# Performance work log

Hardware: AMD Instinct MI355X
Metric: run time of the kernel (lower is better)

The kernel has to match this reference:

```python
import jax, jax.numpy as jnp
import numpy as np

N = 50000   # nodes
E = 800000  # edges
D = 64      # attrs_dim
H = 128     # 2*attrs_dim (GIN MLP hidden)
L = 3       # gnn_layers_num
G = 128     # graphs in batch


def setup_inputs() -> dict:
    key = jax.random.key(0)
    ks = jax.random.split(key, 9)
    s = 0.1
    attrs = jax.random.normal(ks[0], (N, D), dtype=jnp.float32)
    edge_index = jax.random.randint(ks[1], (2, E), 0, N, dtype=jnp.int64)
    batch = jnp.sort(jax.random.randint(ks[2], (N,), 0, G, dtype=jnp.int64))
    W1 = jax.random.normal(ks[3], (L, D, H), dtype=jnp.float32) * s
    b1 = jnp.zeros((L, H), jnp.float32)
    W2 = jax.random.normal(ks[4], (L, H, H), dtype=jnp.float32) * s
    b2 = jnp.zeros((L, H), jnp.float32)
    W3 = jax.random.normal(ks[5], (L, H, D), dtype=jnp.float32) * s
    b3 = jnp.zeros((L, D), jnp.float32)
    return {"attrs": attrs, "W1": W1, "b1": b1, "W2": W2, "b2": b2,
            "W3": W3, "b3": b3, "edge_index": edge_index, "batch": batch}


def reference(attrs, W1, b1, W2, b2, W3, b3, edge_index, batch):
    src, dst = edge_index[0], edge_index[1]
    x = attrs
    for l in range(L):  # small fixed layer count
        # GINConv with eps=0: MLP(x + sum_{j->i} x_j)
        agg = jax.ops.segment_sum(x[src], dst, num_segments=N)
        h = x + agg
        # MLP with tanh after each linear (per MLP.forward)
        h = jnp.tanh(h @ W1[l] + b1[l])
        h = jnp.tanh(h @ W2[l] + b2[l])
        h = jnp.tanh(h @ W3[l] + b3[l])
        # outer activation in GNN.forward
        x = jnp.tanh(h)
    # scatter_mean over graph ids
    sums = jax.ops.segment_sum(x, batch, num_segments=G)          # [G, D]
    counts = jax.ops.segment_sum(jnp.ones((N,), x.dtype), batch, num_segments=G)
    return sums / jnp.maximum(counts, 1.0)[:, None]
```

## Files before the change

### kernel.cpp

```cpp
#include <hip/hip_runtime.h>
#include <math.h>

#define N_NODES 50000
#define N_EDGES 800000
#define DIM 64
#define HID 128
#define LAYERS 3
#define NGRAPH 128

#define SCAN_TILE 1024
#define SCAN_NB ((N_NODES + SCAN_TILE - 1) / SCAN_TILE)

#define POOL_ROWS 256
#define POOL_NB ((N_NODES + POOL_ROWS - 1) / POOL_ROWS)

typedef __attribute__((ext_vector_type(8))) short short8v;
typedef __attribute__((ext_vector_type(4))) float f32x4;

__device__ __forceinline__ float bf2f(unsigned short u) {
    return __uint_as_float(((unsigned)u) << 16);
}
__device__ __forceinline__ unsigned short f2bf(float x) {
    unsigned u = __float_as_uint(x);
    unsigned r = (u + 0x7fff + ((u >> 16) & 1)) >> 16;
    return (unsigned short)r;
}
__device__ __forceinline__ float fast_tanh(float x) {
    float xc = fminf(fmaxf(x, -9.0f), 9.0f);
    float y = __expf(2.0f * xc);
    return 1.0f - 2.0f * __builtin_amdgcn_rcpf(y + 1.0f);
}

__global__ void count_kernel(const int* __restrict__ dst,
                             int* __restrict__ counts,
                             int* __restrict__ rank) {
    int e = blockIdx.x * blockDim.x + threadIdx.x;
    if (e >= N_EDGES) return;
    rank[e] = atomicAdd(&counts[dst[e]], 1);
}

__global__ void scan_partial_kernel(const int* __restrict__ counts,
                                    int* __restrict__ bsum) {
    __shared__ int red[256];
    const int b = blockIdx.x, tid = threadIdx.x;
    const int base = b * SCAN_TILE + tid * 4;
    int s = 0;
    if (base + 3 < N_NODES) {
        int4 v = *reinterpret_cast<const int4*>(counts + base);
        s = v.x + v.y + v.z + v.w;
    } else {
        for (int i = 0; i < 4; ++i)
            if (base + i < N_NODES) s += counts[base + i];
    }
    red[tid] = s;
    __syncthreads();
    for (int off = 128; off > 0; off >>= 1) {
        if (tid < off) red[tid] += red[tid + off];
        __syncthreads();
    }
    if (tid == 0) bsum[b] = red[0];
}

__global__ void scan_mid_kernel(const int* __restrict__ bsum,
                                int* __restrict__ bpre,
                                int* __restrict__ offsets) {
    int tid = threadIdx.x;
    int orig = (tid < SCAN_NB) ? bsum[tid] : 0;
    int v = orig;
    for (int off = 1; off < 64; off <<= 1) {
        int u = __shfl_up(v, off);
        if (tid >= off) v += u;
    }
    if (tid < SCAN_NB) bpre[tid] = v - orig;
    if (tid == 0) offsets[N_NODES] = N_EDGES;
}

__global__ void scan_final_kernel(const int* __restrict__ counts,
                                  const int* __restrict__ bpre,
                                  int* __restrict__ offsets) {
    __shared__ int pre[256];
    const int b = blockIdx.x, tid = threadIdx.x;
    const int base = b * SCAN_TILE + tid * 4;
    int c[4];
    int s = 0;
#pragma unroll
    for (int i = 0; i < 4; ++i) {
        c[i] = (base + i < N_NODES) ? counts[base + i] : 0;
        s += c[i];
    }
    pre[tid] = s;
    __syncthreads();
    for (int off = 1; off < 256; off <<= 1) {
        int v = (tid >= off) ? pre[tid - off] : 0;
        __syncthreads();
        pre[tid] += v;
        __syncthreads();
    }
    int run = bpre[b] + pre[tid] - s;
#pragma unroll
    for (int i = 0; i < 4; ++i) {
        if (base + i < N_NODES) {
            offsets[base + i] = run;
            run += c[i];
        }
    }
}

__global__ void place_kernel(const int* __restrict__ src,
                             const int* __restrict__ dst,
                             const int* __restrict__ rank,
                             const int* __restrict__ offsets,
                             unsigned short* __restrict__ csr_src) {
    int e = blockIdx.x * blockDim.x + threadIdx.x;
    if (e >= N_EDGES) return;
    csr_src[offsets[dst[e]] + rank[e]] = (unsigned short)src[e];
}

template<int K, int C>
__global__ void repack_kernel(const float* __restrict__ W, unsigned short* __restrict__ P) {
    constexpr int KT = K / 32, CT = C / 16;
    int t = blockIdx.x * 256 + threadIdx.x;
    if (t >= LAYERS * KT * CT * 64) return;
    int lane = t & 63; int rest = t >> 6;
    int ct = rest % CT; rest /= CT;
    int kt = rest % KT; int l = rest / KT;
    int li = lane & 15, hi = lane >> 4;
    const float* Wl = W + (size_t)l * K * C;
    short8v o;
#pragma unroll
    for (int j = 0; j < 8; ++j)
        o[j] = (short)f2bf(Wl[(size_t)(kt * 32 + hi * 8 + j) * C + ct * 16 + li]);
    *reinterpret_cast<short8v*>(P + ((size_t)l * KT * CT * 64 + (size_t)(kt * CT + ct) * 64 + lane) * 8) = o;
}

template<bool F32IN>
__global__ __launch_bounds__(256) void gnn_layer_kernel(
        const float* __restrict__ xf, const unsigned short* __restrict__ xb,
        const int* __restrict__ offsets, const unsigned short* __restrict__ csr_src,
        const unsigned short* __restrict__ pw1, const float* __restrict__ bias1,
        const unsigned short* __restrict__ pw2, const float* __restrict__ bias2,
        const unsigned short* __restrict__ pw3, const float* __restrict__ bias3,
        unsigned short* __restrict__ outx) {
    __shared__ unsigned short agg[16 * 64];
    __shared__ unsigned short tileA[16 * 128];
    __shared__ unsigned short tileB[16 * 128];
    const int tid = threadIdx.x;
    const int wave = tid >> 6, lane = tid & 63;
    const int li = lane & 15, hi = lane >> 4;
    const int r0 = blockIdx.x * 16;
    char* tG = reinterpret_cast<char*>(agg);
    char* tA = reinterpret_cast<char*>(tileA);
    char* tB = reinterpret_cast<char*>(tileB);

    {
        const int nr = tid >> 4;
        const int q  = tid & 15;
        const int n  = r0 + nr;
        float a0, a1, a2, a3;
        if (F32IN) {
            float4 v = *reinterpret_cast<const float4*>(xf + (size_t)n * DIM + q * 4);
            a0 = v.x; a1 = v.y; a2 = v.z; a3 = v.w;
        } else {
            ushort4 v = *reinterpret_cast<const ushort4*>(xb + (size_t)n * DIM + q * 4);
            a0 = bf2f(v.x); a1 = bf2f(v.y); a2 = bf2f(v.z); a3 = bf2f(v.w);
        }
        int p = offsets[n];
        const int pe = offsets[n + 1];
        for (; p + 4 <= pe; p += 4) {
            int s0 = csr_src[p + 0];
            int s1 = csr_src[p + 1];
            int s2 = csr_src[p + 2];
            int s3 = csr_src[p + 3];
            if (F32IN) {
                float4 v0 = *reinterpret_cast<const float4*>(xf + (size_t)s0 * DIM + q * 4);
                float4 v1 = *reinterpret_cast<const float4*>(xf + (size_t)s1 * DIM + q * 4);
                float4 v2 = *reinterpret_cast<const float4*>(xf + (size_t)s2 * DIM + q * 4);
                float4 v3 = *reinterpret_cast<const float4*>(xf + (size_t)s3 * DIM + q * 4);
                a0 += v0.x + v1.x + v2.x + v3.x;
                a1 += v0.y + v1.y + v2.y + v3.y;
                a2 += v0.z + v1.z + v2.z + v3.z;
                a3 += v0.w + v1.w + v2.w + v3.w;
            } else {
                ushort4 v0 = *reinterpret_cast<const ushort4*>(xb + (size_t)s0 * DIM + q * 4);
                ushort4 v1 = *reinterpret_cast<const ushort4*>(xb + (size_t)s1 * DIM + q * 4);
                ushort4 v2 = *reinterpret_cast<const ushort4*>(xb + (size_t)s2 * DIM + q * 4);
                ushort4 v3 = *reinterpret_cast<const ushort4*>(xb + (size_t)s3 * DIM + q * 4);
                a0 += bf2f(v0.x) + bf2f(v1.x) + bf2f(v2.x) + bf2f(v3.x);
                a1 += bf2f(v0.y) + bf2f(v1.y) + bf2f(v2.y) + bf2f(v3.y);
                a2 += bf2f(v0.z) + bf2f(v1.z) + bf2f(v2.z) + bf2f(v3.z);
                a3 += bf2f(v0.w) + bf2f(v1.w) + bf2f(v2.w) + bf2f(v3.w);
            }
        }
        for (; p < pe; ++p) {
            int s = csr_src[p];
            if (F32IN) {
                float4 v = *reinterpret_cast<const float4*>(xf + (size_t)s * DIM + q * 4);
                a0 += v.x; a1 += v.y; a2 += v.z; a3 += v.w;
            } else {
                ushort4 v = *reinterpret_cast<const ushort4*>(xb + (size_t)s * DIM + q * 4);
                a0 += bf2f(v.x); a1 += bf2f(v.y); a2 += bf2f(v.z); a3 += bf2f(v.w);
            }
        }
        ushort4 o;
        o.x = f2bf(a0); o.y = f2bf(a1); o.z = f2bf(a2); o.w = f2bf(a3);
        unsigned off = (unsigned)(nr * 128 + q * 8) ^ ((unsigned)(nr & 7) << 4);
        *reinterpret_cast<ushort4*>(tG + off) = o;
    }
    __syncthreads();

    short8v af[2];
#pragma unroll
    for (int kt = 0; kt < 2; ++kt) {
        unsigned off = (unsigned)(li * 128 + (kt * 32 + hi * 8) * 2) ^ ((unsigned)(li & 7) << 4);
        af[kt] = *reinterpret_cast<const short8v*>(tG + off);
    }

    f32x4 acc1[2];
#pragma unroll
    for (int c = 0; c < 2; ++c) acc1[c] = (f32x4){0.f, 0.f, 0.f, 0.f};
#pragma unroll
    for (int c = 0; c < 2; ++c) {
        const int ct = 2 * wave + c;
#pragma unroll
        for (int kt = 0; kt < 2; ++kt) {
            short8v bfr = *reinterpret_cast<const short8v*>(pw1 + ((size_t)(kt * 8 + ct) * 64 + lane) * 8);
            acc1[c] = __builtin_amdgcn_mfma_f32_16x16x32_bf16(af[kt], bfr, acc1[c], 0, 0, 0);
        }
    }
#pragma unroll
    for (int c = 0; c < 2; ++c) {
        const int ct = 2 * wave + c;
        float bv = bias1[ct * 16 + li];
#pragma unroll
        for (int j = 0; j < 4; ++j) {
            int row = hi * 4 + j;
            unsigned off = (unsigned)(row * 256 + (ct * 16 + li) * 2) ^ ((unsigned)(row & 7) << 4);
            *reinterpret_cast<unsigned short*>(tA + off) = f2bf(fast_tanh(acc1[c][j] + bv));
        }
    }
    __syncthreads();

    short8v af2[4];
#pragma unroll
    for (int kt = 0; kt < 4; ++kt) {
        unsigned off = (unsigned)(li * 256 + (kt * 32 + hi * 8) * 2) ^ ((unsigned)(li & 7) << 4);
        af2[kt] = *reinterpret_cast<const short8v*>(tA + off);
    }
    f32x4 acc2[2];
#pragma unroll
    for (int c = 0; c < 2; ++c) acc2[c] = (f32x4){0.f, 0.f, 0.f, 0.f};
#pragma unroll
    for (int c = 0; c < 2; ++c) {
        const int ct = 2 * wave + c;
#pragma unroll
        for (int kt = 0; kt < 4; ++kt) {
            short8v bfr = *reinterpret_cast<const short8v*>(pw2 + ((size_t)(kt * 8 + ct) * 64 + lane) * 8);
            acc2[c] = __builtin_amdgcn_mfma_f32_16x16x32_bf16(af2[kt], bfr, acc2[c], 0, 0, 0);
        }
    }
#pragma unroll
    for (int c = 0; c < 2; ++c) {
        const int ct = 2 * wave + c;
        float bv = bias2[ct * 16 + li];
#pragma unroll
        for (int j = 0; j < 4; ++j) {
            int row = hi * 4 + j;
            unsigned off = (unsigned)(row * 256 + (ct * 16 + li) * 2) ^ ((unsigned)(row & 7) << 4);
            *reinterpret_cast<unsigned short*>(tB + off) = f2bf(fast_tanh(acc2[c][j] + bv));
        }
    }
    __syncthreads();

    short8v af3[4];
#pragma unroll
    for (int kt = 0; kt < 4; ++kt) {
        unsigned off = (unsigned)(li * 256 + (kt * 32 + hi * 8) * 2) ^ ((unsigned)(li & 7) << 4);
        af3[kt] = *reinterpret_cast<const short8v*>(tB + off);
    }
    f32x4 acc3 = (f32x4){0.f, 0.f, 0.f, 0.f};
#pragma unroll
    for (int kt = 0; kt < 4; ++kt) {
        short8v bfr = *reinterpret_cast<const short8v*>(pw3 + ((size_t)(kt * 4 + wave) * 64 + lane) * 8);
        acc3 = __builtin_amdgcn_mfma_f32_16x16x32_bf16(af3[kt], bfr, acc3, 0, 0, 0);
    }
    {
        float bv = bias3[wave * 16 + li];
#pragma unroll
        for (int j = 0; j < 4; ++j) {
            int row = r0 + hi * 4 + j;
            float v = fast_tanh(fast_tanh(acc3[j] + bv));
            outx[(size_t)row * DIM + wave * 16 + li] = f2bf(v);
        }
    }
}

__global__ void pool_partial_kernel(const unsigned short* __restrict__ x,
                                    const int* __restrict__ batch,
                                    float* __restrict__ sums) {
    const int tid = threadIdx.x;
    const int d = tid & 63;
    const int rg = tid >> 6;
    int row = blockIdx.x * POOL_ROWS + rg;
    const int rowend = min(N_NODES, (blockIdx.x + 1) * POOL_ROWS);
    float acc = 0.f;
    int cur = -1;
    for (; row < rowend; row += 4) {
        int g = batch[row];
        if (g != cur) {
            if (cur >= 0) atomicAdd(&sums[cur * DIM + d], acc);
            acc = 0.f;
            cur = g;
        }
        acc += bf2f(x[(size_t)row * DIM + d]);
    }
    if (cur >= 0) atomicAdd(&sums[cur * DIM + d], acc);
}

__global__ void pool_final_kernel(const float* __restrict__ sums,
                                  const int* __restrict__ batch,
                                  float* __restrict__ out) {
    const int g = blockIdx.x;
    const int d = threadIdx.x;
    int lo = 0, hi = N_NODES;
    while (lo < hi) { int m = (lo + hi) >> 1; if (batch[m] < g) lo = m + 1; else hi = m; }
    int start = lo;
    hi = N_NODES;
    while (lo < hi) { int m = (lo + hi) >> 1; if (batch[m] < g + 1) lo = m + 1; else hi = m; }
    float cnt = (float)(lo - start);
    out[g * DIM + d] = sums[g * DIM + d] / fmaxf(cnt, 1.f);
}

extern "C" void kernel_launch(void* const* d_in, const int* in_sizes, int n_in,
                              void* d_out, int out_size, void* d_ws, size_t ws_size,
                              hipStream_t stream) {
    const float* attrs = (const float*)d_in[0];
    const float* W1    = (const float*)d_in[1];
    const float* b1    = (const float*)d_in[2];
    const float* W2    = (const float*)d_in[3];
    const float* b2    = (const float*)d_in[4];
    const float* W3    = (const float*)d_in[5];
    const float* b3    = (const float*)d_in[6];
    const int* edge_index = (const int*)d_in[7];
    const int* batch      = (const int*)d_in[8];
    float* out = (float*)d_out;

    unsigned short* buf0 = (unsigned short*)d_ws;
    unsigned short* buf1 = buf0 + (size_t)N_NODES * DIM;
    unsigned short* pW1  = buf1 + (size_t)N_NODES * DIM;
    unsigned short* pW2  = pW1 + 24576;
    unsigned short* pW3  = pW2 + 49152;
    float* psums  = (float*)(pW3 + 24576);
    int* offsets  = (int*)(psums + NGRAPH * DIM);
    unsigned short* csr16 = (unsigned short*)(offsets + N_NODES + 1);
    int* rank     = (int*)(csr16 + N_EDGES);
    int* counts   = rank + N_EDGES;
    int* bsum     = counts + N_NODES;
    int* bpre     = bsum + SCAN_NB;

    const int* src = edge_index;
    const int* dst = edge_index + N_EDGES;

    const int edge_blocks = (N_EDGES + 255) / 256;
    const int gnn_blocks  = N_NODES / 16;

    hipMemsetAsync(counts, 0, (size_t)N_NODES * sizeof(int), stream);
    count_kernel<<<edge_blocks, 256, 0, stream>>>(dst, counts, rank);
    scan_partial_kernel<<<SCAN_NB, 256, 0, stream>>>(counts, bsum);
    scan_mid_kernel<<<1, 64, 0, stream>>>(bsum, bpre, offsets);
    scan_final_kernel<<<SCAN_NB, 256, 0, stream>>>(counts, bpre, offsets);
    place_kernel<<<edge_blocks, 256, 0, stream>>>(src, dst, rank, offsets, csr16);

    repack_kernel<DIM, HID><<<(LAYERS * 2 * 8 * 64 + 255) / 256, 256, 0, stream>>>(W1, pW1);
    repack_kernel<HID, HID><<<(LAYERS * 4 * 8 * 64 + 255) / 256, 256, 0, stream>>>(W2, pW2);
    repack_kernel<HID, DIM><<<(LAYERS * 4 * 4 * 64 + 255) / 256, 256, 0, stream>>>(W3, pW3);

    for (int l = 0; l < LAYERS; ++l) {
        const unsigned short* w1 = pW1 + (size_t)l * 2 * 8 * 64 * 8;
        const unsigned short* w2 = pW2 + (size_t)l * 4 * 8 * 64 * 8;
        const unsigned short* w3 = pW3 + (size_t)l * 4 * 4 * 64 * 8;
        const float* bb1 = b1 + (size_t)l * HID;
        const float* bb2 = b2 + (size_t)l * HID;
        const float* bb3 = b3 + (size_t)l * DIM;
        if (l == 0)
            gnn_layer_kernel<true><<<gnn_blocks, 256, 0, stream>>>(
                attrs, nullptr, offsets, csr16, w1, bb1, w2, bb2, w3, bb3, buf0);
        else {
            const unsigned short* in = (l == 1) ? buf0 : buf1;
            unsigned short* outb     = (l == 1) ? buf1 : buf0;
            gnn_layer_kernel<false><<<gnn_blocks, 256, 0, stream>>>(
                nullptr, in, offsets, csr16, w1, bb1, w2, bb2, w3, bb3, outb);
        }
    }

    hipMemsetAsync(psums, 0, (size_t)NGRAPH * DIM * sizeof(float), stream);
    pool_partial_kernel<<<POOL_NB, 256, 0, stream>>>(buf0, batch, psums);
    pool_final_kernel<<<NGRAPH, DIM, 0, stream>>>(psums, batch, out);
}
```

Before: 192.8 us.

## Balance edge aggregation across a block's rows with LDS float atomics

Measured after the change: 269.3 us. +39.7%, slower.

```diff
diff --git a/kernel.cpp b/kernel.cpp
--- a/kernel.cpp
+++ b/kernel.cpp
@@ -33,10 +33,10 @@
 
 __global__ void count_kernel(const int* __restrict__ dst,
                              int* __restrict__ counts,
-                             int* __restrict__ rank) {
+                             unsigned short* __restrict__ rank) {
     int e = blockIdx.x * blockDim.x + threadIdx.x;
     if (e >= N_EDGES) return;
-    rank[e] = atomicAdd(&counts[dst[e]], 1);
+    rank[e] = (unsigned short)atomicAdd(&counts[dst[e]], 1);
 }
 
 __global__ void scan_partial_kernel(const int* __restrict__ counts,
@@ -108,12 +108,12 @@
 
 __global__ void place_kernel(const int* __restrict__ src,
                              const int* __restrict__ dst,
-                             const int* __restrict__ rank,
+                             const unsigned short* __restrict__ rank,
                              const int* __restrict__ offsets,
                              unsigned short* __restrict__ csr_src) {
     int e = blockIdx.x * blockDim.x + threadIdx.x;
     if (e >= N_EDGES) return;
-    csr_src[offsets[dst[e]] + rank[e]] = (unsigned short)src[e];
+    csr_src[offsets[dst[e]] + (int)rank[e]] = (unsigned short)src[e];
 }
 
 template<int K, int C>
@@ -141,78 +141,106 @@
         const unsigned short* __restrict__ pw2, const float* __restrict__ bias2,
         const unsigned short* __restrict__ pw3, const float* __restrict__ bias3,
         unsigned short* __restrict__ outx) {
-    __shared__ unsigned short agg[16 * 64];
+    __shared__ float aggF[16 * 68];
     __shared__ unsigned short tileA[16 * 128];
     __shared__ unsigned short tileB[16 * 128];
+    __shared__ int soff[17];
     const int tid = threadIdx.x;
     const int wave = tid >> 6, lane = tid & 63;
     const int li = lane & 15, hi = lane >> 4;
     const int r0 = blockIdx.x * 16;
-    char* tG = reinterpret_cast<char*>(agg);
     char* tA = reinterpret_cast<char*>(tileA);
     char* tB = reinterpret_cast<char*>(tileB);
 
+    if (tid < 17) soff[tid] = offsets[r0 + tid];
+
     {
-        const int nr = tid >> 4;
-        const int q  = tid & 15;
-        const int n  = r0 + nr;
-        float a0, a1, a2, a3;
+        const int nr = tid >> 4, q = tid & 15;
+        const int n = r0 + nr;
+        float v0, v1, v2, v3;
         if (F32IN) {
             float4 v = *reinterpret_cast<const float4*>(xf + (size_t)n * DIM + q * 4);
-            a0 = v.x; a1 = v.y; a2 = v.z; a3 = v.w;
+            v0 = v.x; v1 = v.y; v2 = v.z; v3 = v.w;
         } else {
-            ushort4 v = *reinterpret_cast<const ushort4*>(xb + (size_t)n * DIM + q * 4);
-            a0 = bf2f(v.x); a1 = bf2f(v.y); a2 = bf2f(v.z); a3 = bf2f(v.w);
-        }
-        int p = offsets[n];
-        const int pe = offsets[n + 1];
-        for (; p + 4 <= pe; p += 4) {
-            int s0 = csr_src[p + 0];
-            int s1 = csr_src[p + 1];
-            int s2 = csr_src[p + 2];
-            int s3 = csr_src[p + 3];
-            if (F32IN) {
-                float4 v0 = *reinterpret_cast<const float4*>(xf + (size_t)s0 * DIM + q * 4);
-                float4 v1 = *reinterpret_cast<const float4*>(xf + (size_t)s1 * DIM + q * 4);
-                float4 v2 = *reinterpret_cast<const float4*>(xf + (size_t)s2 * DIM + q * 4);
-                float4 v3 = *reinterpret_cast<const float4*>(xf + (size_t)s3 * DIM + q * 4);
-                a0 += v0.x + v1.x + v2.x + v3.x;
-                a1 += v0.y + v1.y + v2.y + v3.y;
-                a2 += v0.z + v1.z + v2.z + v3.z;
-                a3 += v0.w + v1.w + v2.w + v3.w;
-            } else {
-                ushort4 v0 = *reinterpret_cast<const ushort4*>(xb + (size_t)s0 * DIM + q * 4);
-                ushort4 v1 = *reinterpret_cast<const ushort4*>(xb + (size_t)s1 * DIM + q * 4);
-                ushort4 v2 = *reinterpret_cast<const ushort4*>(xb + (size_t)s2 * DIM + q * 4);
-                ushort4 v3 = *reinterpret_cast<const ushort4*>(xb + (size_t)s3 * DIM + q * 4);
-                a0 += bf2f(v0.x) + bf2f(v1.x) + bf2f(v2.x) + bf2f(v3.x);
-                a1 += bf2f(v0.y) + bf2f(v1.y) + bf2f(v2.y) + bf2f(v3.y);
-                a2 += bf2f(v0.z) + bf2f(v1.z) + bf2f(v2.z) + bf2f(v3.z);
-                a3 += bf2f(v0.w) + bf2f(v1.w) + bf2f(v2.w) + bf2f(v3.w);
+            ushort4 u = *reinterpret_cast<const ushort4*>(xb + (size_t)n * DIM + q * 4);
+            v0 = bf2f(u.x); v1 = bf2f(u.y); v2 = bf2f(u.z); v3 = bf2f(u.w);
+        }
+        float* d = &aggF[nr * 68 + q * 4];
+        d[0] = v0; d[1] = v1; d[2] = v2; d[3] = v3;
+    }
+    __syncthreads();
+
+    {
+        const int g = tid >> 4, q = tid & 15;
+        const int pb = soff[0];
+        const int pend = soff[16];
+        const int m = pend - pb;
+        const int chunk = (m + 15) >> 4;
+        int p = pb + g * chunk;
+        const int pe = min(p + chunk, pend);
+        if (p < pe) {
+            int row = 0;
+            while (soff[row + 1] <= p) ++row;
+            int next = soff[row + 1];
+            float a0 = 0.f, a1 = 0.f, a2 = 0.f, a3 = 0.f;
+            while (p < pe) {
+                if (p >= next) {
+                    float* d = &aggF[row * 68 + q * 4];
+                    atomicAdd(d + 0, a0); atomicAdd(d + 1, a1);
+                    atomicAdd(d + 2, a2); atomicAdd(d + 3, a3);
+                    a0 = a1 = a2 = a3 = 0.f;
+                    do { ++row; next = soff[row + 1]; } while (p >= next);
+                }
+                const int lim = min(pe, next);
+                for (; p + 4 <= lim; p += 4) {
+                    int s0 = csr_src[p + 0];
+                    int s1 = csr_src[p + 1];
+                    int s2 = csr_src[p + 2];
+                    int s3 = csr_src[p + 3];
+                    if (F32IN) {
+                        float4 v0 = *reinterpret_cast<const float4*>(xf + (size_t)s0 * DIM + q * 4);
+                        float4 v1 = *reinterpret_cast<const float4*>(xf + (size_t)s1 * DIM + q * 4);
+                        float4 v2 = *reinterpret_cast<const float4*>(xf + (size_t)s2 * DIM + q * 4);
+                        float4 v3 = *reinterpret_cast<const float4*>(xf + (size_t)s3 * DIM + q * 4);
+                        a0 += v0.x + v1.x + v2.x + v3.x;
+                        a1 += v0.y + v1.y + v2.y + v3.y;
+                        a2 += v0.z + v1.z + v2.z + v3.z;
+                        a3 += v0.w + v1.w + v2.w + v3.w;
+                    } else {
+                        ushort4 v0 = *reinterpret_cast<const ushort4*>(xb + (size_t)s0 * DIM + q * 4);
+                        ushort4 v1 = *reinterpret_cast<const ushort4*>(xb + (size_t)s1 * DIM + q * 4);
+                        ushort4 v2 = *reinterpret_cast<const ushort4*>(xb + (size_t)s2 * DIM + q * 4);
+                        ushort4 v3 = *reinterpret_cast<const ushort4*>(xb + (size_t)s3 * DIM + q * 4);
+                        a0 += bf2f(v0.x) + bf2f(v1.x) + bf2f(v2.x) + bf2f(v3.x);
+                        a1 += bf2f(v0.y) + bf2f(v1.y) + bf2f(v2.y) + bf2f(v3.y);
+                        a2 += bf2f(v0.z) + bf2f(v1.z) + bf2f(v2.z) + bf2f(v3.z);
+                        a3 += bf2f(v0.w) + bf2f(v1.w) + bf2f(v2.w) + bf2f(v3.w);
+                    }
+                }
+                for (; p < lim; ++p) {
+                    int s = csr_src[p];
+                    if (F32IN) {
+                        float4 v = *reinterpret_cast<const float4*>(xf + (size_t)s * DIM + q * 4);
+                        a0 += v.x; a1 += v.y; a2 += v.z; a3 += v.w;
+                    } else {
+                        ushort4 v = *reinterpret_cast<const ushort4*>(xb + (size_t)s * DIM + q * 4);
+                        a0 += bf2f(v.x); a1 += bf2f(v.y); a2 += bf2f(v.z); a3 += bf2f(v.w);
+                    }
+                }
             }
-        }
-        for (; p < pe; ++p) {
-            int s = csr_src[p];
-            if (F32IN) {
-                float4 v = *reinterpret_cast<const float4*>(xf + (size_t)s * DIM + q * 4);
-                a0 += v.x; a1 += v.y; a2 += v.z; a3 += v.w;
-            } else {
-                ushort4 v = *reinterpret_cast<const ushort4*>(xb + (size_t)s * DIM + q * 4);
-                a0 += bf2f(v.x); a1 += bf2f(v.y); a2 += bf2f(v.z); a3 += bf2f(v.w);
-            }
-        }
-        ushort4 o;
-        o.x = f2bf(a0); o.y = f2bf(a1); o.z = f2bf(a2); o.w = f2bf(a3);
-        unsigned off = (unsigned)(nr * 128 + q * 8) ^ ((unsigned)(nr & 7) << 4);
-        *reinterpret_cast<ushort4*>(tG + off) = o;
+            float* d = &aggF[row * 68 + q * 4];
+            atomicAdd(d + 0, a0); atomicAdd(d + 1, a1);
+            atomicAdd(d + 2, a2); atomicAdd(d + 3, a3);
+        }
     }
     __syncthreads();
 
     short8v af[2];
 #pragma unroll
     for (int kt = 0; kt < 2; ++kt) {
-        unsigned off = (unsigned)(li * 128 + (kt * 32 + hi * 8) * 2) ^ ((unsigned)(li & 7) << 4);
-        af[kt] = *reinterpret_cast<const short8v*>(tG + off);
+        const float* s = &aggF[li * 68 + kt * 32 + hi * 8];
+#pragma unroll
+        for (int j = 0; j < 8; ++j) af[kt][j] = (short)f2bf(s[j]);
     }
 
     f32x4 acc1[2];
@@ -352,8 +380,8 @@
     float* psums  = (float*)(pW3 + 24576);
     int* offsets  = (int*)(psums + NGRAPH * DIM);
     unsigned short* csr16 = (unsigned short*)(offsets + N_NODES + 1);
-    int* rank     = (int*)(csr16 + N_EDGES);
-    int* counts   = rank + N_EDGES;
+    unsigned short* rank  = csr16 + N_EDGES;
+    int* counts   = (int*)(rank + N_EDGES);
     int* bsum     = counts + N_NODES;
     int* bpre     = bsum + SCAN_NB;
 
```

## Split neighbor aggregation across two thread groups per node with wider loads

Applied to the files above, without the earlier changes.

Result: faster. 186.7 us (-3.1%).

```diff
diff --git a/kernel.cpp b/kernel.cpp
--- a/kernel.cpp
+++ b/kernel.cpp
@@ -33,10 +33,10 @@
 
 __global__ void count_kernel(const int* __restrict__ dst,
                              int* __restrict__ counts,
-                             int* __restrict__ rank) {
+                             unsigned short* __restrict__ rank) {
     int e = blockIdx.x * blockDim.x + threadIdx.x;
     if (e >= N_EDGES) return;
-    rank[e] = atomicAdd(&counts[dst[e]], 1);
+    rank[e] = (unsigned short)atomicAdd(&counts[dst[e]], 1);
 }
 
 __global__ void scan_partial_kernel(const int* __restrict__ counts,
@@ -108,12 +108,12 @@
 
 __global__ void place_kernel(const int* __restrict__ src,
                              const int* __restrict__ dst,
-                             const int* __restrict__ rank,
+                             const unsigned short* __restrict__ rank,
                              const int* __restrict__ offsets,
                              unsigned short* __restrict__ csr_src) {
     int e = blockIdx.x * blockDim.x + threadIdx.x;
     if (e >= N_EDGES) return;
-    csr_src[offsets[dst[e]] + rank[e]] = (unsigned short)src[e];
+    csr_src[offsets[dst[e]] + (int)rank[e]] = (unsigned short)src[e];
 }
 
 template<int K, int C>
@@ -141,78 +141,112 @@
         const unsigned short* __restrict__ pw2, const float* __restrict__ bias2,
         const unsigned short* __restrict__ pw3, const float* __restrict__ bias3,
         unsigned short* __restrict__ outx) {
-    __shared__ unsigned short agg[16 * 64];
+    __shared__ float aggA[16 * 68];
+    __shared__ float aggB[16 * 68];
     __shared__ unsigned short tileA[16 * 128];
     __shared__ unsigned short tileB[16 * 128];
+    __shared__ int soff[17];
     const int tid = threadIdx.x;
     const int wave = tid >> 6, lane = tid & 63;
     const int li = lane & 15, hi = lane >> 4;
     const int r0 = blockIdx.x * 16;
-    char* tG = reinterpret_cast<char*>(agg);
     char* tA = reinterpret_cast<char*>(tileA);
     char* tB = reinterpret_cast<char*>(tileB);
 
+    if (tid < 17) soff[tid] = offsets[r0 + tid];
+    __syncthreads();
+
     {
-        const int nr = tid >> 4;
-        const int q  = tid & 15;
+        const int g  = tid >> 3;
+        const int nr = g >> 1;
+        const int h  = g & 1;
+        const int q  = tid & 7;
         const int n  = r0 + nr;
-        float a0, a1, a2, a3;
-        if (F32IN) {
-            float4 v = *reinterpret_cast<const float4*>(xf + (size_t)n * DIM + q * 4);
-            a0 = v.x; a1 = v.y; a2 = v.z; a3 = v.w;
+        float a[8];
+        if (h == 0) {
+            if (F32IN) {
+                const float* xr = xf + (size_t)n * DIM + q * 8;
+                float4 u = *reinterpret_cast<const float4*>(xr);
+                float4 w = *reinterpret_cast<const float4*>(xr + 4);
+                a[0]=u.x; a[1]=u.y; a[2]=u.z; a[3]=u.w;
+                a[4]=w.x; a[5]=w.y; a[6]=w.z; a[7]=w.w;
+            } else {
+                short8v v = *reinterpret_cast<const short8v*>(xb + (size_t)n * DIM + q * 8);
+#pragma unroll
+                for (int j = 0; j < 8; ++j) a[j] = bf2f((unsigned short)v[j]);
+            }
         } else {
-            ushort4 v = *reinterpret_cast<const ushort4*>(xb + (size_t)n * DIM + q * 4);
-            a0 = bf2f(v.x); a1 = bf2f(v.y); a2 = bf2f(v.z); a3 = bf2f(v.w);
-        }
-        int p = offsets[n];
-        const int pe = offsets[n + 1];
+#pragma unroll
+            for (int j = 0; j < 8; ++j) a[j] = 0.f;
+        }
+        const int p0 = soff[nr], pe1 = soff[nr + 1];
+        const int mid = p0 + ((pe1 - p0 + 1) >> 1);
+        int p        = h ? mid : p0;
+        const int pe = h ? pe1 : mid;
         for (; p + 4 <= pe; p += 4) {
             int s0 = csr_src[p + 0];
             int s1 = csr_src[p + 1];
             int s2 = csr_src[p + 2];
             int s3 = csr_src[p + 3];
             if (F32IN) {
-                float4 v0 = *reinterpret_cast<const float4*>(xf + (size_t)s0 * DIM + q * 4);
-                float4 v1 = *reinterpret_cast<const float4*>(xf + (size_t)s1 * DIM + q * 4);
-                float4 v2 = *reinterpret_cast<const float4*>(xf + (size_t)s2 * DIM + q * 4);
-                float4 v3 = *reinterpret_cast<const float4*>(xf + (size_t)s3 * DIM + q * 4);
-                a0 += v0.x + v1.x + v2.x + v3.x;
-                a1 += v0.y + v1.y + v2.y + v3.y;
-                a2 += v0.z + v1.z + v2.z + v3.z;
-                a3 += v0.w + v1.w + v2.w + v3.w;
+                const float* x0 = xf + (size_t)s0 * DIM + q * 8;
+                const float* x1 = xf + (size_t)s1 * DIM + q * 8;
+                const float* x2 = xf + (size_t)s2 * DIM + q * 8;
+                const float* x3 = xf + (size_t)s3 * DIM + q * 8;
+                float4 u0 = *reinterpret_cast<const float4*>(x0);
+                float4 w0 = *reinterpret_cast<const float4*>(x0 + 4);
+                float4 u1 = *reinterpret_cast<const float4*>(x1);
+                float4 w1 = *reinterpret_cast<const float4*>(x1 + 4);
+                float4 u2 = *reinterpret_cast<const float4*>(x2);
+                float4 w2 = *reinterpret_cast<const float4*>(x2 + 4);
+                float4 u3 = *reinterpret_cast<const float4*>(x3);
+                float4 w3 = *reinterpret_cast<const float4*>(x3 + 4);
+                a[0] += u0.x + u1.x + u2.x + u3.x;
+                a[1] += u0.y + u1.y + u2.y + u3.y;
+                a[2] += u0.z + u1.z + u2.z + u3.z;
+                a[3] += u0.w + u1.w + u2.w + u3.w;
+                a[4] += w0.x + w1.x + w2.x + w3.x;
+                a[5] += w0.y + w1.y + w2.y + w3.y;
+                a[6] += w0.z + w1.z + w2.z + w3.z;
+                a[7] += w0.w + w1.w + w2.w + w3.w;
             } else {
-                ushort4 v0 = *reinterpret_cast<const ushort4*>(xb + (size_t)s0 * DIM + q * 4);
-                ushort4 v1 = *reinterpret_cast<const ushort4*>(xb + (size_t)s1 * DIM + q * 4);
-                ushort4 v2 = *reinterpret_cast<const ushort4*>(xb + (size_t)s2 * DIM + q * 4);
-                ushort4 v3 = *reinterpret_cast<const ushort4*>(xb + (size_t)s3 * DIM + q * 4);
-                a0 += bf2f(v0.x) + bf2f(v1.x) + bf2f(v2.x) + bf2f(v3.x);
-                a1 += bf2f(v0.y) + bf2f(v1.y) + bf2f(v2.y) + bf2f(v3.y);
-                a2 += bf2f(v0.z) + bf2f(v1.z) + bf2f(v2.z) + bf2f(v3.z);
-                a3 += bf2f(v0.w) + bf2f(v1.w) + bf2f(v2.w) + bf2f(v3.w);
+                short8v v0 = *reinterpret_cast<const short8v*>(xb + (size_t)s0 * DIM + q * 8);
+                short8v v1 = *reinterpret_cast<const short8v*>(xb + (size_t)s1 * DIM + q * 8);
+                short8v v2 = *reinterpret_cast<const short8v*>(xb + (size_t)s2 * DIM + q * 8);
+                short8v v3 = *reinterpret_cast<const short8v*>(xb + (size_t)s3 * DIM + q * 8);
+#pragma unroll
+                for (int j = 0; j < 8; ++j)
+                    a[j] += bf2f((unsigned short)v0[j]) + bf2f((unsigned short)v1[j])
+                          + bf2f((unsigned short)v2[j]) + bf2f((unsigned short)v3[j]);
             }
         }
         for (; p < pe; ++p) {
             int s = csr_src[p];
             if (F32IN) {
-                float4 v = *reinterpret_cast<const float4*>(xf + (size_t)s * DIM + q * 4);
-                a0 += v.x; a1 += v.y; a2 += v.z; a3 += v.w;
+                const float* xs = xf + (size_t)s * DIM + q * 8;
+                float4 u = *reinterpret_cast<const float4*>(xs);
+                float4 w = *reinterpret_cast<const float4*>(xs + 4);
+                a[0] += u.x; a[1] += u.y; a[2] += u.z; a[3] += u.w;
+                a[4] += w.x; a[5] += w.y; a[6] += w.z; a[7] += w.w;
             } else {
-                ushort4 v = *reinterpret_cast<const ushort4*>(xb + (size_t)s * DIM + q * 4);
-                a0 += bf2f(v.x); a1 += bf2f(v.y); a2 += bf2f(v.z); a3 += bf2f(v.w);
+                short8v v = *reinterpret_cast<const short8v*>(xb + (size_t)s * DIM + q * 8);
+#pragma unroll
+                for (int j = 0; j < 8; ++j) a[j] += bf2f((unsigned short)v[j]);
             }
         }
-        ushort4 o;
-        o.x = f2bf(a0); o.y = f2bf(a1); o.z = f2bf(a2); o.w = f2bf(a3);
-        unsigned off = (unsigned)(nr * 128 + q * 8) ^ ((unsigned)(nr & 7) << 4);
-        *reinterpret_cast<ushort4*>(tG + off) = o;
+        float* d = (h ? aggB : aggA) + nr * 68 + q * 8;
+        *reinterpret_cast<f32x4*>(d)     = (f32x4){a[0], a[1], a[2], a[3]};
+        *reinterpret_cast<f32x4*>(d + 4) = (f32x4){a[4], a[5], a[6], a[7]};
     }
     __syncthreads();
 
     short8v af[2];
 #pragma unroll
     for (int kt = 0; kt < 2; ++kt) {
-        unsigned off = (unsigned)(li * 128 + (kt * 32 + hi * 8) * 2) ^ ((unsigned)(li & 7) << 4);
-        af[kt] = *reinterpret_cast<const short8v*>(tG + off);
+        const float* sA = &aggA[li * 68 + kt * 32 + hi * 8];
+        const float* sB = &aggB[li * 68 + kt * 32 + hi * 8];
+#pragma unroll
+        for (int j = 0; j < 8; ++j) af[kt][j] = (short)f2bf(sA[j] + sB[j]);
     }
 
     f32x4 acc1[2];
@@ -352,8 +386,8 @@
     float* psums  = (float*)(pW3 + 24576);
     int* offsets  = (int*)(psums + NGRAPH * DIM);
     unsigned short* csr16 = (unsigned short*)(offsets + N_NODES + 1);
-    int* rank     = (int*)(csr16 + N_EDGES);
-    int* counts   = rank + N_EDGES;
+    unsigned short* rank  = csr16 + N_EDGES;
+    int* counts   = (int*)(rank + N_EDGES);
     int* bsum     = counts + N_NODES;
     int* bpre     = bsum + SCAN_NB;
 
```
